# Kernel tuning notes

Hardware: AMD Instinct MI355X
Metric: run time of the kernel (lower is better)

Reference implementation:

```python
import jax, jax.numpy as jnp
import numpy as np

B = 131072
DIM = 64
D_IN = 32
D_OUT = 32
HIDDEN = 512
N_BINS = 8
TAIL = 3.0


def setup_inputs() -> dict:
    key = jax.random.key(0)
    ks = jax.random.split(key, 7)
    x = jax.random.normal(ks[0], (B, DIM), dtype=jnp.float32)
    out_dim = D_OUT * (3 * N_BINS - 1)  # 32 * 23 = 736
    W1 = jax.random.normal(ks[1], (D_IN, HIDDEN), dtype=jnp.float32) / np.sqrt(D_IN)
    b1 = jnp.zeros((HIDDEN,), dtype=jnp.float32)
    W2 = jax.random.normal(ks[2], (HIDDEN, HIDDEN), dtype=jnp.float32) / np.sqrt(HIDDEN)
    b2 = jnp.zeros((HIDDEN,), dtype=jnp.float32)
    W3 = jax.random.normal(ks[3], (HIDDEN, out_dim), dtype=jnp.float32) / np.sqrt(HIDDEN)
    b3 = jnp.zeros((out_dim,), dtype=jnp.float32)
    return {"x": x, "W1": W1, "b1": b1, "W2": W2, "b2": b2, "W3": W3, "b3": b3}


def _gather(t, idx):
    # t: (..., K), idx: (...) -> (...,)
    return jnp.take_along_axis(t, idx[..., None], axis=-1)[..., 0]


def rq_spline_forward(x, widths, heights, derivatives, tail_bound=TAIL):
    K = widths.shape[-1]
    widths = jax.nn.softmax(widths, axis=-1) * 2 * tail_bound
    heights = jax.nn.softmax(heights, axis=-1) * 2 * tail_bound
    derivatives = jax.nn.softplus(derivatives)
    ones = jnp.ones_like(derivatives[..., :1])
    derivatives = jnp.concatenate([ones, derivatives, ones], axis=-1)  # (..., K+1)
    cumwidths = jnp.cumsum(widths, axis=-1)
    cumwidths = jnp.pad(cumwidths, [(0, 0)] * (cumwidths.ndim - 1) + [(1, 0)]) - tail_bound
    cumheights = jnp.cumsum(heights, axis=-1)
    cumheights = jnp.pad(cumheights, [(0, 0)] * (cumheights.ndim - 1) + [(1, 0)]) - tail_bound

    inside = (x >= -tail_bound) & (x <= tail_bound)
    xc = jnp.clip(x, -tail_bound + 1e-6, tail_bound - 1e-6)
    # searchsorted (left): number of knots strictly less than xc
    bin_idx = jnp.sum(cumwidths[..., 1:] < xc[..., None], axis=-1)
    bin_idx = jnp.clip(bin_idx, 0, K - 1)

    w_k = _gather(widths, bin_idx)
    h_k = _gather(heights, bin_idx)
    d_k = _gather(derivatives, bin_idx)
    d_k1 = _gather(derivatives[..., 1:], bin_idx)
    cw_k = _gather(cumwidths, bin_idx)
    ch_k = _gather(cumheights, bin_idx)

    xi = jnp.clip((xc - cw_k) / w_k, 1e-6, 1 - 1e-6)
    s_k = h_k / w_k
    num = h_k * (s_k * xi**2 + d_k * xi * (1 - xi))
    den = s_k + (d_k + d_k1 - 2 * s_k) * xi * (1 - xi)
    y_inside = ch_k + num / den
    log_det_inside = (
        jnp.log(s_k**2 * (d_k1 * xi**2 + 2 * s_k * xi * (1 - xi) + d_k * (1 - xi) ** 2) + 1e-8)
        - jnp.log(den**2 + 1e-8)
    )
    y = jnp.where(inside, y_inside, x)
    log_det = jnp.where(inside, log_det_inside, jnp.zeros_like(x))
    return y, log_det


def reference(x, W1, b1, W2, b2, W3, b3):
    # mask: first D_IN dims conditioned on, last D_OUT transformed
    x_masked = x[:, :D_IN]
    x_transform = x[:, D_IN:]
    h = jax.nn.relu(x_masked @ W1 + b1)
    h = jax.nn.relu(h @ W2 + b2)
    raw = h @ W3 + b3
    raw = raw.reshape(x.shape[0], D_OUT, 3 * N_BINS - 1)
    widths = raw[..., :N_BINS]
    heights = raw[..., N_BINS:2 * N_BINS]
    derivs = raw[..., 2 * N_BINS:]
    y_t, log_det = rq_spline_forward(x_transform, widths, heights, derivs, TAIL)
    y = jnp.concatenate([x_masked, y_t], axis=-1)
    return y, jnp.sum(log_det, axis=-1)
```

## Files before the change

kernel.cpp:

```cpp
#include <hip/hip_runtime.h>
#include <hip/hip_bf16.h>
#include <stdint.h>

typedef __bf16 bf16_t;
typedef _Float16 f16_t;
typedef _Float16 f16x8 __attribute__((ext_vector_type(8)));
typedef _Float16 f16x4 __attribute__((ext_vector_type(4)));
typedef float f32x4 __attribute__((ext_vector_type(4)));

#define HID 512
#define NRAW 736
#define NRAW_PAD 768
#define TAILB 3.0f

__device__ __forceinline__ void glds16(const void* g, void* s) {
  __builtin_amdgcn_global_load_lds(
      (const __attribute__((address_space(1))) void*)g,
      (__attribute__((address_space(3))) void*)s, 16, 0, 0);
}
__device__ __forceinline__ float frcp(float x) { return __builtin_amdgcn_rcpf(x); }

__global__ void detect_dtype(const void* x, int* flag) {
  __shared__ int s;
  if (threadIdx.x == 0) s = 0;
  __syncthreads();
  const bf16_t* xb = (const bf16_t*)x;
  int cnt = 0;
  for (int j = 0; j < 16; j++) {
    float v = (float)xb[threadIdx.x * 16 + j];
    if (!(v == v) || fabsf(v) > 64.0f) cnt++;
  }
  atomicAdd(&s, cnt);
  __syncthreads();
  if (threadIdx.x == 0) *flag = (s > 64) ? 1 : 0;
}

__global__ void conv_wb(const void* W1, const void* W2, const void* W3,
                        const void* b1, const void* b2, const void* b3,
                        f16_t* __restrict__ w1t, f16_t* __restrict__ w2t,
                        f16_t* __restrict__ w3t,
                        float* __restrict__ bf1, float* __restrict__ bf2,
                        float* __restrict__ bf3, const int* flagp) {
  const int flag = *flagp;
  auto rd = [&](const void* p, size_t idx) -> float {
    return flag ? ((const float*)p)[idx] : (float)((const bf16_t*)p)[idx];
  };
  int i = blockIdx.x * 256 + threadIdx.x;
  if (i < 512 * 32)  { w1t[i] = (f16_t)rd(W1, (size_t)(i & 31) * 512 + (i >> 5)); return; }
  i -= 512 * 32;
  if (i < 512 * 512) { w2t[i] = (f16_t)rd(W2, (size_t)(i & 511) * 512 + (i >> 9)); return; }
  i -= 512 * 512;
  if (i < NRAW_PAD * 512) {
    int n = i >> 9, k = i & 511;
    int ch = n / 24, e = n % 24;
    w3t[i] = (e < 23) ? (f16_t)rd(W3, (size_t)k * NRAW + ch * 23 + e) : (f16_t)0.0f;
    return;
  }
  i -= NRAW_PAD * 512;
  if (i < 512) { bf1[i] = rd(b1, i); return; }
  i -= 512;
  if (i < 512) { bf2[i] = rd(b2, i); return; }
  i -= 512;
  if (i < NRAW_PAD) {
    int ch = i / 24, e = i % 24;
    bf3[i] = (e < 23) ? rd(b3, (size_t)ch * 23 + e) : 0.0f;
  }
}

__global__ void convert_x(const void* x, void* __restrict__ outv,
                          const int* flagp, int n) {
  const int flag = *flagp;
  const int i0 = (blockIdx.x * 256 + threadIdx.x) * 8;
  if (i0 >= n) return;
  const int row = i0 >> 5, col = i0 & 31;
  const size_t src = (size_t)row * 64 + col;
  if (flag) {
    const float4* s4 = (const float4*)((const float*)x + src);
    float4* d4 = (float4*)((float*)outv + src);
    d4[0] = s4[0]; d4[1] = s4[1];
  } else {
    *(uint4*)((bf16_t*)outv + src) = *(const uint4*)((const bf16_t*)x + src);
  }
}

__global__ void ld_finalize(const float* __restrict__ ldp, void* __restrict__ outv,
                            const int* __restrict__ flagp, int M) {
  const int i = blockIdx.x * 256 + threadIdx.x;
  if (i >= M) return;
  float s = 0.f;
  #pragma unroll
  for (int n = 0; n < 4; n++) s += ldp[(size_t)n * M + i];
  if (*flagp) ((float*)outv)[(size_t)M * 64 + i] = s;
  else        ((bf16_t*)outv)[(size_t)M * 64 + i] = (bf16_t)s;
}

__launch_bounds__(256)
__global__ void gemm12(const void* __restrict__ xorig, const f16_t* __restrict__ W1t,
                       const float* __restrict__ b1, const f16_t* __restrict__ W2t,
                       const float* __restrict__ b2, f16_t* __restrict__ H2,
                       int r0, const int* __restrict__ flagp) {
  constexpr int BK = 64;
  __shared__ __align__(16) f16_t As[128 * BK], Bs[128 * BK];
  const int t = threadIdx.x;
  const int id = blockIdx.x;
  const int xcd = id & 7, s = id >> 3;
  const int n0 = (s & 3) * 128;
  const int m0 = ((s >> 2) * 8 + xcd) * 128;
  const int lrow = t >> 3, lcb = t & 7;
  const int lane = t & 63, w = t >> 6;
  const int wr = (w >> 1) * 64, wc = (w & 1) * 64, wc2 = (w & 1) * 32;
  const int lm = lane & 15, quad = lane >> 4;
  const int flag = *flagp;

  const f16_t* gb[4];
  f16_t* ldb[4];
  #pragma unroll
  for (int r = 0; r < 4; r++) {
    const int row = r * 32 + lrow;
    const int gc = (lcb ^ (row & 7)) * 8;
    gb[r] = W2t + (size_t)(n0 + row) * 512 + gc;
    ldb[r] = &Bs[row * BK + lcb * 8];
  }
  const f16x8* ap[4][2];
  const f16x8* bp[4][2];
  #pragma unroll
  for (int i = 0; i < 4; i++) {
    const int ra = wr + i * 16 + lm, rb = wc + i * 16 + lm;
    #pragma unroll
    for (int ksi = 0; ksi < 2; ksi++) {
      const int qb = ksi * 4 + quad;
      ap[i][ksi] = (const f16x8*)&As[ra * BK + ((qb ^ (ra & 7)) << 3)];
      bp[i][ksi] = (const f16x8*)&Bs[rb * BK + ((qb ^ (rb & 7)) << 3)];
    }
  }
  f16x8 xfr[4];
  #pragma unroll
  for (int i = 0; i < 4; i++) {
    const size_t xrow = (size_t)(r0 + m0 + wr + i * 16 + lm);
    if (flag) {
      const float* px = (const float*)xorig + xrow * 64 + quad * 8;
      const float4 a = *(const float4*)px;
      const float4 b = *(const float4*)(px + 4);
      f16x8 v;
      v[0] = (f16_t)a.x; v[1] = (f16_t)a.y; v[2] = (f16_t)a.z; v[3] = (f16_t)a.w;
      v[4] = (f16_t)b.x; v[5] = (f16_t)b.y; v[6] = (f16_t)b.z; v[7] = (f16_t)b.w;
      xfr[i] = v;
    } else {
      const bf16_t* px = (const bf16_t*)xorig + xrow * 64 + quad * 8;
      f16x8 v;
      #pragma unroll
      for (int j = 0; j < 8; j++) v[j] = (f16_t)(float)px[j];
      xfr[i] = v;
    }
  }
  const f16_t* w1p0 = W1t + (size_t)(wc2 + lm) * 32 + quad * 8;
  const f16_t* w1p1 = W1t + (size_t)(wc2 + 16 + lm) * 32 + quad * 8;
  const float* b1p0 = b1 + wc2 + 4 * quad;
  const float* b1p1 = b1 + wc2 + 16 + 4 * quad;
  f16_t* wadr[4][2];
  #pragma unroll
  for (int i = 0; i < 4; i++) {
    const int row = wr + i * 16 + lm;
    #pragma unroll
    for (int Tl = 0; Tl < 2; Tl++) {
      const int cb = (wc2 >> 3) + 2 * Tl + (quad >> 1);
      wadr[i][Tl] = &As[row * BK + ((cb ^ (row & 7)) << 3) + 4 * (quad & 1)];
    }
  }

  f32x4 acc[4][4] = {};
  f16x8 w1f0 = *(const f16x8*)w1p0;
  f16x8 w1f1 = *(const f16x8*)w1p1;

  #pragma unroll
  for (int k0i = 0; k0i < 8; k0i++) {
    const int k0 = k0i * 64;
    #pragma unroll
    for (int r = 0; r < 4; r++) glds16(gb[r] + k0, ldb[r]);
    const float4 bv0 = *(const float4*)(b1p0 + k0);
    const float4 bv1 = *(const float4*)(b1p1 + k0);
    f32x4 h[4][2];
    #pragma unroll
    for (int i = 0; i < 4; i++) {
      f32x4 z = {};
      h[i][0] = __builtin_amdgcn_mfma_f32_16x16x32_f16(w1f0, xfr[i], z, 0, 0, 0);
      h[i][1] = __builtin_amdgcn_mfma_f32_16x16x32_f16(w1f1, xfr[i], z, 0, 0, 0);
    }
    if (k0i < 7) {
      w1f0 = *(const f16x8*)(w1p0 + (size_t)(k0 + 64) * 32);
      w1f1 = *(const f16x8*)(w1p1 + (size_t)(k0 + 64) * 32);
    }
    __syncthreads();
    #pragma unroll
    for (int i = 0; i < 4; i++) {
      f16x4 v0, v1;
      v0[0] = (f16_t)fmaxf(h[i][0][0] + bv0.x, 0.0f);
      v0[1] = (f16_t)fmaxf(h[i][0][1] + bv0.y, 0.0f);
      v0[2] = (f16_t)fmaxf(h[i][0][2] + bv0.z, 0.0f);
      v0[3] = (f16_t)fmaxf(h[i][0][3] + bv0.w, 0.0f);
      v1[0] = (f16_t)fmaxf(h[i][1][0] + bv1.x, 0.0f);
      v1[1] = (f16_t)fmaxf(h[i][1][1] + bv1.y, 0.0f);
      v1[2] = (f16_t)fmaxf(h[i][1][2] + bv1.z, 0.0f);
      v1[3] = (f16_t)fmaxf(h[i][1][3] + bv1.w, 0.0f);
      *(f16x4*)wadr[i][0] = v0;
      *(f16x4*)wadr[i][1] = v1;
    }
    __syncthreads();
    #pragma unroll
    for (int ksi = 0; ksi < 2; ksi++) {
      f16x8 af[4], bf[4];
      #pragma unroll
      for (int i = 0; i < 4; i++) af[i] = *ap[i][ksi];
      #pragma unroll
      for (int j = 0; j < 4; j++) bf[j] = *bp[j][ksi];
      #pragma unroll
      for (int i = 0; i < 4; i++)
        #pragma unroll
        for (int j = 0; j < 4; j++)
          acc[i][j] = __builtin_amdgcn_mfma_f32_16x16x32_f16(af[i], bf[j], acc[i][j], 0, 0, 0);
    }
    if (k0i < 7) __syncthreads();
  }
  #pragma unroll
  for (int i = 0; i < 4; i++)
    #pragma unroll
    for (int j = 0; j < 4; j++) {
      const int col = n0 + wc + j * 16 + lm;
      const float bv = b2[col];
      #pragma unroll
      for (int r = 0; r < 4; r++) {
        const int rowi = m0 + wr + i * 16 + quad * 4 + r;
        H2[(size_t)rowi * HID + col] = (f16_t)fmaxf(acc[i][j][r] + bv, 0.0f);
      }
    }
}

#define RSH 200
#define SP1 0.5413248546f

__launch_bounds__(512, 2)
__global__ void gemm3_spline(const f16_t* __restrict__ A, const f16_t* __restrict__ Bt,
                             const float* __restrict__ bias,
                             const void* __restrict__ xorig,
                             void* __restrict__ outv, float* __restrict__ ldp,
                             int M, int r0, const int* __restrict__ flagp) {
  __shared__ __align__(16) f16_t lds[2 * 16384 + 2 * 12288];
  f16_t* As = lds;
  f16_t* Bs = lds + 2 * 16384;
  f16_t* rawh = lds;

  const int t = threadIdx.x;
  const int id = blockIdx.x;
  const int xcd = id & 7, sloc = id >> 3;
  const int cpx = gridDim.x >> 3;
  const int wg = xcd * cpx + sloc;
  const int ntile = wg & 3;
  const int m0 = (wg >> 2) * 256;
  const int n0 = ntile * 192;
  const int lane = t & 63, w = t >> 6;
  const int lm = lane & 15, quad = lane >> 4;
  const int wrow = (w >> 2) * 128, wcol = (w & 3) * 48;
  const int lrow = t >> 3, lcb = t & 7;
  const int flag = *flagp;

  const int gc = (lcb ^ (lrow & 7)) * 8;
  const f16_t* gA = A + (size_t)(m0 + lrow) * 512 + gc;
  const f16_t* gB = Bt + (size_t)(n0 + lrow) * 512 + gc;
  f16_t* ldA = As + lrow * 64 + lcb * 8;
  f16_t* ldB = Bs + lrow * 64 + lcb * 8;

  int aoff[8], boff[3];
  #pragma unroll
  for (int i = 0; i < 8; i++) {
    const int ra = wrow + i * 16 + lm;
    aoff[i] = ra * 64 + ((quad ^ (ra & 7)) << 3);
  }
  #pragma unroll
  for (int j = 0; j < 3; j++) {
    const int rb = wcol + j * 16 + lm;
    boff[j] = rb * 64 + ((quad ^ (rb & 7)) << 3);
  }

  #pragma unroll
  for (int r = 0; r < 4; r++) glds16(gA + r * 32768, ldA + r * 4096);
  #pragma unroll
  for (int r = 0; r < 3; r++) glds16(gB + r * 32768, ldB + r * 4096);

  const int prow = t >> 3, pch = t & 7;
  float xt_pre[4];
  #pragma unroll
  for (int e = 0; e < 4; e++) {
    const size_t gi = (size_t)(r0 + m0 + e * 64 + prow) * 64 + 32 + ntile * 8 + pch;
    xt_pre[e] = flag ? ((const float*)xorig)[gi] : (float)((const bf16_t*)xorig)[gi];
  }
  float bv3[3];
  #pragma unroll
  for (int j = 0; j < 3; j++) bv3[j] = bias[n0 + wcol + j * 16 + lm];

  asm volatile("s_waitcnt vmcnt(0)" ::: "memory");
  __builtin_amdgcn_sched_barrier(0);
  __builtin_amdgcn_s_barrier();

  f32x4 acc[8][3] = {};

  #pragma unroll
  for (int t8 = 0; t8 < 8; t8++) {
    const f16_t* Ab = As + (t8 & 1) * 16384;
    const f16_t* Bb = Bs + (t8 & 1) * 12288;
    f16_t* ldAn = ldA + ((t8 + 1) & 1) * 16384;
    f16_t* ldBn = ldB + ((t8 + 1) & 1) * 12288;
    const f16_t* gAn = gA + (t8 + 1) * 64;
    const f16_t* gBn = gB + (t8 + 1) * 64;

    #pragma unroll
    for (int p = 0; p < 4; p++) {
      const int ksi = p >> 1, rh = p & 1;
      f16x8 af[4], bf[3];
      #pragma unroll
      for (int ii = 0; ii < 4; ii++)
        af[ii] = *(const f16x8*)(Ab + (aoff[rh * 4 + ii] ^ (ksi << 5)));
      #pragma unroll
      for (int j = 0; j < 3; j++)
        bf[j] = *(const f16x8*)(Bb + (boff[j] ^ (ksi << 5)));
      if (t8 < 7) {
        if (p == 0) {
          #pragma unroll
          for (int r = 0; r < 4; r++) glds16(gAn + r * 32768, ldAn + r * 4096);
        } else if (p == 1) {
          #pragma unroll
          for (int r = 0; r < 3; r++) glds16(gBn + r * 32768, ldBn + r * 4096);
        }
      }
      __builtin_amdgcn_s_barrier();
      __builtin_amdgcn_s_setprio(1);
      #pragma unroll
      for (int ii = 0; ii < 4; ii++)
        #pragma unroll
        for (int j = 0; j < 3; j++)
          acc[rh * 4 + ii][j] = __builtin_amdgcn_mfma_f32_16x16x32_f16(
              af[ii], bf[j], acc[rh * 4 + ii][j], 0, 0, 0);
      __builtin_amdgcn_s_setprio(0);
    }
    if (t8 < 7) {
      asm volatile("s_waitcnt vmcnt(0)" ::: "memory");
      __builtin_amdgcn_sched_barrier(0);
      __builtin_amdgcn_s_barrier();
    }
  }

  __syncthreads();

  #pragma unroll
  for (int i = 0; i < 8; i++)
    #pragma unroll
    for (int j = 0; j < 3; j++) {
      const int col = wcol + j * 16 + lm;
      #pragma unroll
      for (int r = 0; r < 4; r++)
        rawh[(wrow + i * 16 + quad * 4 + r) * RSH + col] = (f16_t)(acc[i][j][r] + bv3[j]);
    }
  __syncthreads();

  #pragma unroll
  for (int e = 0; e < 4; e++) {
    const int row = e * 64 + prow;
    const f16_t* c16 = &rawh[row * RSH + pch * 24];
    const f16x8 v0 = *(const f16x8*)(c16);
    const f16x8 v1 = *(const f16x8*)(c16 + 8);
    const f16x8 v2 = *(const f16x8*)(c16 + 16);
    float wa[8], ha[8], da[7];
    #pragma unroll
    for (int j = 0; j < 8; j++) { wa[j] = (float)v0[j]; ha[j] = (float)v1[j]; }
    #pragma unroll
    for (int j = 0; j < 7; j++) da[j] = (float)v2[j];

    const float xt = xt_pre[e];
    const bool inside = (xt >= -TAILB) && (xt <= TAILB);
    const float xc = fminf(fmaxf(xt, -TAILB + 1e-6f), TAILB - 1e-6f);

    float mw = wa[0], mh = ha[0];
    #pragma unroll
    for (int j = 1; j < 8; j++) { mw = fmaxf(mw, wa[j]); mh = fmaxf(mh, ha[j]); }
    float ew[8], eh[8], sew = 0.f, seh = 0.f;
    #pragma unroll
    for (int j = 0; j < 8; j++) {
      ew[j] = __expf(wa[j] - mw); sew += ew[j];
      eh[j] = __expf(ha[j] - mh); seh += eh[j];
    }
    const float wsc = 6.0f * frcp(sew), hsc = 6.0f * frcp(seh);
    #pragma unroll
    for (int j = 0; j < 8; j++) { ew[j] *= wsc; eh[j] *= hsc; }

    float accw = -TAILB, runh = -TAILB;
    float cwk = -TAILB, chk = -TAILB;
    float wk = ew[0], hk = eh[0];
    float dkr = SP1, dk1r = da[0];
    #pragma unroll
    for (int i = 0; i < 7; i++) {
      accw += ew[i];
      runh += eh[i];
      const bool cond = accw < xc;
      cwk  = cond ? accw : cwk;
      chk  = cond ? runh : chk;
      wk   = cond ? ew[i + 1] : wk;
      hk   = cond ? eh[i + 1] : hk;
      dkr  = cond ? da[i] : dkr;
      dk1r = cond ? ((i == 6) ? SP1 : da[i + 1]) : dk1r;
    }
    const float dk  = fmaxf(dkr, 0.0f)  + __logf(1.0f + __expf(-fabsf(dkr)));
    const float dk1 = fmaxf(dk1r, 0.0f) + __logf(1.0f + __expf(-fabsf(dk1r)));

    const float rwk = frcp(wk);
    float xi = (xc - cwk) * rwk;
    xi = fminf(fmaxf(xi, 1e-6f), 1.0f - 1e-6f);
    const float om = 1.0f - xi;
    const float sl = hk * rwk;
    const float num = hk * (sl * xi * xi + dk * xi * om);
    const float den = sl + (dk + dk1 - 2.0f * sl) * xi * om;
    const float y_in = chk + num * frcp(den);
    const float t1 = sl * sl * (dk1 * xi * xi + 2.0f * sl * xi * om + dk * om * om);
    const float ld_in = __logf(t1 + 1e-8f) - __logf(den * den + 1e-8f);

    const float yv = inside ? y_in : xt;
    const float ldv = inside ? ld_in : 0.0f;

    const size_t grow = (size_t)(r0 + m0 + row);
    if (flag) ((float*)outv)[grow * 64 + 32 + ntile * 8 + pch] = yv;
    else      ((bf16_t*)outv)[grow * 64 + 32 + ntile * 8 + pch] = (bf16_t)yv;

    float l = ldv + __shfl_down(ldv, 1, 8);
    l += __shfl_down(l, 2, 8);
    l += __shfl_down(l, 4, 8);
    if ((t & 7) == 0) ldp[(size_t)ntile * M + grow] = l;
  }
}

extern "C" void kernel_launch(void* const* d_in, const int* in_sizes, int n_in,
                              void* d_out, int out_size, void* d_ws, size_t ws_size,
                              hipStream_t stream) {
  const void* x  = d_in[0];
  const void* W1 = d_in[1];
  const void* b1 = d_in[2];
  const void* W2 = d_in[3];
  const void* b2 = d_in[4];
  const void* W3 = d_in[5];
  const void* b3 = d_in[6];
  const int M = in_sizes[0] / 64;

  char* ws = (char*)d_ws;
  size_t off = 0;
  auto alloc = [&](size_t bytes) {
    void* p = ws + off;
    off += (bytes + 255) & ~(size_t)255;
    return p;
  };
  int*   flag = (int*)alloc(256);
  float* bf1  = (float*)alloc(512 * 4);
  float* bf2  = (float*)alloc(512 * 4);
  float* bf3  = (float*)alloc(NRAW_PAD * 4);
  f16_t* W1t  = (f16_t*)alloc((size_t)512 * 32 * 2);
  f16_t* W2t  = (f16_t*)alloc((size_t)512 * 512 * 2);
  f16_t* W3t  = (f16_t*)alloc((size_t)NRAW_PAD * 512 * 2);
  float* ldp  = (float*)alloc((size_t)8 * M * 4);

  const size_t per_row = (size_t)HID * 2;
  size_t avail = (ws_size > off + 4096) ? (ws_size - off - 4096) : 0;
  long rows = (long)(avail / per_row);
  rows -= rows % 1024;
  if (rows > M) rows = M;
  if (rows < 1024) rows = 1024;

  f16_t* h2 = (f16_t*)alloc((size_t)rows * HID * 2);

  detect_dtype<<<1, 256, 0, stream>>>(x, flag);
  conv_wb<<<2631, 256, 0, stream>>>(W1, W2, W3, b1, b2, b3,
                                    W1t, W2t, W3t, bf1, bf2, bf3, flag);
  convert_x<<<(M * 32 / 8 + 255) / 256, 256, 0, stream>>>(x, d_out, flag, M * 32);

  for (int r0 = 0; r0 < M; r0 += (int)rows) {
    const int mc = (int)((M - r0 < rows) ? (M - r0) : rows);
    const int mt128 = mc / 128;
    const int mt256 = mc / 256;
    gemm12<<<mt128 * 4, 256, 0, stream>>>(x, W1t, bf1, W2t, bf2, h2, r0, flag);
    gemm3_spline<<<mt256 * 4, 512, 0, stream>>>(
        h2, W3t, bf3, x, d_out, ldp, M, r0, flag);
  }
  ld_finalize<<<(M + 255) / 256, 256, 0, stream>>>(ldp, d_out, flag, M);
}
```

Before: 356.7 us.

## Halve gemm3_spline M-tile to 128 rows and simplify the double-buffered K loop

The fused GEMM3+spline kernel now handles 128 rows per block instead of 256. This halves the A-tile LDS buffers, the accumulators and the per-thread spline work, and launches twice as many blocks. The intent is more resident blocks per CU (launch bounds raised to 4) and better latency hiding. The K loop also changes: the fine per-phase barriers and explicit vmcnt waits are gone, the next tile is prefetched at the start of each iteration, and a single __syncthreads closes it. The cost is that each W3 tile is loaded twice as often, and completion of the async global-to-LDS loads now relies on __syncthreads.

```diff
diff --git a/kernel.cpp b/kernel.cpp
--- a/kernel.cpp
+++ b/kernel.cpp
@@ -238,15 +238,15 @@
 #define RSH 200
 #define SP1 0.5413248546f
 
-__launch_bounds__(512, 2)
+__launch_bounds__(512, 4)
 __global__ void gemm3_spline(const f16_t* __restrict__ A, const f16_t* __restrict__ Bt,
                              const float* __restrict__ bias,
                              const void* __restrict__ xorig,
                              void* __restrict__ outv, float* __restrict__ ldp,
                              int M, int r0, const int* __restrict__ flagp) {
-  __shared__ __align__(16) f16_t lds[2 * 16384 + 2 * 12288];
+  __shared__ __align__(16) f16_t lds[2 * 8192 + 2 * 12288];
   f16_t* As = lds;
-  f16_t* Bs = lds + 2 * 16384;
+  f16_t* Bs = lds + 2 * 8192;
   f16_t* rawh = lds;
 
   const int t = threadIdx.x;
@@ -255,11 +255,11 @@
   const int cpx = gridDim.x >> 3;
   const int wg = xcd * cpx + sloc;
   const int ntile = wg & 3;
-  const int m0 = (wg >> 2) * 256;
+  const int m0 = (wg >> 2) * 128;
   const int n0 = ntile * 192;
   const int lane = t & 63, w = t >> 6;
   const int lm = lane & 15, quad = lane >> 4;
-  const int wrow = (w >> 2) * 128, wcol = (w & 3) * 48;
+  const int wrow = (w >> 2) * 64, wcol = (w & 3) * 48;
   const int lrow = t >> 3, lcb = t & 7;
   const int flag = *flagp;
 
@@ -269,9 +269,9 @@
   f16_t* ldA = As + lrow * 64 + lcb * 8;
   f16_t* ldB = Bs + lrow * 64 + lcb * 8;
 
-  int aoff[8], boff[3];
-  #pragma unroll
-  for (int i = 0; i < 8; i++) {
+  int aoff[4], boff[3];
+  #pragma unroll
+  for (int i = 0; i < 4; i++) {
     const int ra = wrow + i * 16 + lm;
     aoff[i] = ra * 64 + ((quad ^ (ra & 7)) << 3);
   }
@@ -281,15 +281,10 @@
     boff[j] = rb * 64 + ((quad ^ (rb & 7)) << 3);
   }
 
-  #pragma unroll
-  for (int r = 0; r < 4; r++) glds16(gA + r * 32768, ldA + r * 4096);
-  #pragma unroll
-  for (int r = 0; r < 3; r++) glds16(gB + r * 32768, ldB + r * 4096);
-
   const int prow = t >> 3, pch = t & 7;
-  float xt_pre[4];
-  #pragma unroll
-  for (int e = 0; e < 4; e++) {
+  float xt_pre[2];
+  #pragma unroll
+  for (int e = 0; e < 2; e++) {
     const size_t gi = (size_t)(r0 + m0 + e * 64 + prow) * 64 + 32 + ntile * 8 + pch;
     xt_pre[e] = flag ? ((const float*)xorig)[gi] : (float)((const bf16_t*)xorig)[gi];
   }
@@ -297,61 +292,49 @@
   #pragma unroll
   for (int j = 0; j < 3; j++) bv3[j] = bias[n0 + wcol + j * 16 + lm];
 
-  asm volatile("s_waitcnt vmcnt(0)" ::: "memory");
-  __builtin_amdgcn_sched_barrier(0);
-  __builtin_amdgcn_s_barrier();
-
-  f32x4 acc[8][3] = {};
+  #pragma unroll
+  for (int r = 0; r < 2; r++) glds16(gA + r * 32768, ldA + r * 4096);
+  #pragma unroll
+  for (int r = 0; r < 3; r++) glds16(gB + r * 32768, ldB + r * 4096);
+  __syncthreads();
+
+  f32x4 acc[4][3] = {};
 
   #pragma unroll
   for (int t8 = 0; t8 < 8; t8++) {
-    const f16_t* Ab = As + (t8 & 1) * 16384;
+    const f16_t* Ab = As + (t8 & 1) * 8192;
     const f16_t* Bb = Bs + (t8 & 1) * 12288;
-    f16_t* ldAn = ldA + ((t8 + 1) & 1) * 16384;
-    f16_t* ldBn = ldB + ((t8 + 1) & 1) * 12288;
-    const f16_t* gAn = gA + (t8 + 1) * 64;
-    const f16_t* gBn = gB + (t8 + 1) * 64;
-
-    #pragma unroll
-    for (int p = 0; p < 4; p++) {
-      const int ksi = p >> 1, rh = p & 1;
+    if (t8 < 7) {
+      const int nb = (t8 + 1) & 1;
+      #pragma unroll
+      for (int r = 0; r < 2; r++)
+        glds16(gA + r * 32768 + (t8 + 1) * 64, ldA + nb * 8192 + r * 4096);
+      #pragma unroll
+      for (int r = 0; r < 3; r++)
+        glds16(gB + r * 32768 + (t8 + 1) * 64, ldB + nb * 12288 + r * 4096);
+    }
+    #pragma unroll
+    for (int ksi = 0; ksi < 2; ksi++) {
       f16x8 af[4], bf[3];
       #pragma unroll
-      for (int ii = 0; ii < 4; ii++)
-        af[ii] = *(const f16x8*)(Ab + (aoff[rh * 4 + ii] ^ (ksi << 5)));
+      for (int i = 0; i < 4; i++)
+        af[i] = *(const f16x8*)(Ab + (aoff[i] ^ (ksi << 5)));
       #pragma unroll
       for (int j = 0; j < 3; j++)
         bf[j] = *(const f16x8*)(Bb + (boff[j] ^ (ksi << 5)));
-      if (t8 < 7) {
-        if (p == 0) {
-          #pragma unroll
-          for (int r = 0; r < 4; r++) glds16(gAn + r * 32768, ldAn + r * 4096);
-        } else if (p == 1) {
-          #pragma unroll
-          for (int r = 0; r < 3; r++) glds16(gBn + r * 32768, ldBn + r * 4096);
-        }
-      }
-      __builtin_amdgcn_s_barrier();
       __builtin_amdgcn_s_setprio(1);
       #pragma unroll
-      for (int ii = 0; ii < 4; ii++)
+      for (int i = 0; i < 4; i++)
         #pragma unroll
         for (int j = 0; j < 3; j++)
-          acc[rh * 4 + ii][j] = __builtin_amdgcn_mfma_f32_16x16x32_f16(
-              af[ii], bf[j], acc[rh * 4 + ii][j], 0, 0, 0);
+          acc[i][j] = __builtin_amdgcn_mfma_f32_16x16x32_f16(af[i], bf[j], acc[i][j], 0, 0, 0);
       __builtin_amdgcn_s_setprio(0);
     }
-    if (t8 < 7) {
-      asm volatile("s_waitcnt vmcnt(0)" ::: "memory");
-      __builtin_amdgcn_sched_barrier(0);
-      __builtin_amdgcn_s_barrier();
-    }
-  }
-
-  __syncthreads();
-
-  #pragma unroll
-  for (int i = 0; i < 8; i++)
+    __syncthreads();
+  }
+
+  #pragma unroll
+  for (int i = 0; i < 4; i++)
     #pragma unroll
     for (int j = 0; j < 3; j++) {
       const int col = wcol + j * 16 + lm;
@@ -362,7 +345,7 @@
   __syncthreads();
 
   #pragma unroll
-  for (int e = 0; e < 4; e++) {
+  for (int e = 0; e < 2; e++) {
     const int row = e * 64 + prow;
     const f16_t* c16 = &rawh[row * RSH + pch * 24];
     const f16x8 v0 = *(const f16x8*)(c16);
@@ -480,9 +463,8 @@
   for (int r0 = 0; r0 < M; r0 += (int)rows) {
     const int mc = (int)((M - r0 < rows) ? (M - r0) : rows);
     const int mt128 = mc / 128;
-    const int mt256 = mc / 256;
     gemm12<<<mt128 * 4, 256, 0, stream>>>(x, W1t, bf1, W2t, bf2, h2, r0, flag);
-    gemm3_spline<<<mt256 * 4, 512, 0, stream>>>(
+    gemm3_spline<<<mt128 * 4, 512, 0, stream>>>(
         h2, W3t, bf3, x, d_out, ldp, M, r0, flag);
   }
   ld_finalize<<<(M + 255) / 256, 256, 0, stream>>>(ldp, d_out, flag, M);
```

Measured after the change: 327.0 us. 8.3% less time.
